# Performance work log

Hardware: AMD Instinct MI355X
Metric: run time of the kernel (lower is better)

## Reference

```python
import jax, jax.numpy as jnp
import numpy as np
import math

N_HEADS = 16


def _rope(t, cos, sin):
    # t: [B, S, H, d_k] with d_k paired as (even, odd) -> complex multiply by cos+i*sin
    B, S, H, dk = t.shape
    t = t.reshape(B, S, H, dk // 2, 2)
    t0, t1 = t[..., 0], t[..., 1]
    c = cos[None, :S, None, :]
    s = sin[None, :S, None, :]
    out = jnp.stack([t0 * c - t1 * s, t0 * s + t1 * c], axis=-1)
    return out.reshape(B, S, H, dk)


def setup_inputs() -> dict:
    key = jax.random.key(0)
    ks = jax.random.split(key, 6)
    B, S, D = 2, 2048, 2048
    dk = D // N_HEADS  # 128
    x = jax.random.normal(ks[0], (B, S, D), dtype=jnp.float32)
    # standard RoPE angle table
    inv_freq = 1.0 / (10000.0 ** (np.arange(0, dk, 2, dtype=np.float32) / dk))  # [dk/2]
    t = np.arange(S, dtype=np.float32)
    ang = np.outer(t, inv_freq)  # [S, dk/2]
    freqs_cos = jnp.asarray(np.cos(ang), dtype=jnp.float32)
    freqs_sin = jnp.asarray(np.sin(ang), dtype=jnp.float32)
    # additive causal mask [1,1,S,S]
    causal = jnp.tril(jnp.ones((S, S), dtype=bool))
    mask = jnp.where(causal, 0.0, -1e9).astype(jnp.float32)[None, None]
    wscale = 1.0 / math.sqrt(D)
    Wq = jax.random.normal(ks[1], (D, D), dtype=jnp.float32) * wscale
    Wk = jax.random.normal(ks[2], (D, D), dtype=jnp.float32) * wscale
    Wv = jax.random.normal(ks[3], (D, D), dtype=jnp.float32) * wscale
    Wo = jax.random.normal(ks[4], (D, D), dtype=jnp.float32) * wscale
    return {"x": x, "freqs_cos": freqs_cos, "freqs_sin": freqs_sin, "mask": mask,
            "Wq": Wq, "Wk": Wk, "Wv": Wv, "Wo": Wo}


def reference(x, freqs_cos, freqs_sin, mask, Wq, Wk, Wv, Wo):
    B, S, D = x.shape
    H = N_HEADS
    dk = D // H
    scale = math.sqrt(dk)
    # nn.Linear(w) applies x @ w.T
    Q = (x @ Wq.T).reshape(B, S, H, dk)
    K = (x @ Wk.T).reshape(B, S, H, dk)
    V = (x @ Wv.T).reshape(B, S, H, dk)
    Q = _rope(Q, freqs_cos, freqs_sin)
    K = _rope(K, freqs_cos, freqs_sin)
    new_kv_cache = (K, V)  # kv_cache=None path: cache is just current K, V
    # [B, H, S, dk]
    Qh = Q.transpose(0, 2, 1, 3)
    Kh = K.transpose(0, 2, 1, 3)
    Vh = V.transpose(0, 2, 1, 3)
    scores = jnp.einsum('bhqd,bhkd->bhqk', Qh, Kh) / scale + mask
    attn = jax.nn.softmax(scores, axis=-1)  # dropout=0 (eval)
    ctx = jnp.einsum('bhqk,bhkd->bhqd', attn, Vh)
    ctx = ctx.transpose(0, 2, 1, 3).reshape(B, S, D)
    output = ctx @ Wo.T
    return output, new_kv_cache[0], new_kv_cache[1]
```

## Files before the change

kernel.cpp:

```cpp
#include <hip/hip_runtime.h>
#include <hip/hip_bf16.h>

#define SEQ   2048
#define DIM   2048
#define NH    16
#define DKH   128
#define BATCH 2
#define MROWS (BATCH * SEQ)
#define NQT   (SEQ / 64)

using bf16 = __hip_bfloat16;
typedef __attribute__((ext_vector_type(8))) short short8;
typedef __attribute__((ext_vector_type(4))) short short4v;
typedef __attribute__((ext_vector_type(4))) float floatx4;

union BfBits { bf16 h; short s; };

__device__ __forceinline__ void gl_lds16(const bf16* g, bf16* l) {
  __builtin_amdgcn_global_load_lds(
      (__attribute__((address_space(1))) void*)(g),
      (__attribute__((address_space(3))) void*)(l), 16, 0, 0);
}

__global__ __launch_bounds__(256) void cast_kernel(const float* __restrict__ src,
                                                   bf16* __restrict__ dst, int n4) {
  int i = blockIdx.x * 256 + threadIdx.x;
  if (i >= n4) return;
  float4 v = reinterpret_cast<const float4*>(src)[i];
  __hip_bfloat162 h01, h23;
  h01.x = __float2bfloat16(v.x); h01.y = __float2bfloat16(v.y);
  h23.x = __float2bfloat16(v.z); h23.y = __float2bfloat16(v.w);
  reinterpret_cast<__hip_bfloat162*>(dst)[i * 2 + 0] = h01;
  reinterpret_cast<__hip_bfloat162*>(dst)[i * 2 + 1] = h23;
}

template <typename CT>
__global__ __launch_bounds__(256) void gemm_bt(const bf16* __restrict__ A,
                                               const bf16* __restrict__ Bw,
                                               CT* __restrict__ C,
                                               int M, int N, int K) {
  __shared__ bf16 As[128 * 32];
  __shared__ bf16 Bs[128 * 32];
  const int t = threadIdx.x;
  const int m0 = blockIdx.y * 128;
  const int n0 = blockIdx.x * 128;
  const int w = t >> 6, lane = t & 63;
  const int wm = (w >> 1) * 64, wn = (w & 1) * 64;
  const int lr = lane & 15, quad = lane >> 4;

  const int c0 = w * 2;
  const int r0 = lane >> 2;
  const int kc = (lane & 3) * 8;

  floatx4 acc[4][4];
#pragma unroll
  for (int i = 0; i < 4; ++i)
#pragma unroll
    for (int j = 0; j < 4; ++j)
      acc[i][j] = (floatx4){0.f, 0.f, 0.f, 0.f};

  for (int k0 = 0; k0 < K; k0 += 32) {
    gl_lds16(A + (size_t)(m0 + c0 * 16 + r0) * K + k0 + kc,       As + c0 * 512);
    gl_lds16(A + (size_t)(m0 + (c0 + 1) * 16 + r0) * K + k0 + kc, As + (c0 + 1) * 512);
    gl_lds16(Bw + (size_t)(n0 + c0 * 16 + r0) * K + k0 + kc,       Bs + c0 * 512);
    gl_lds16(Bw + (size_t)(n0 + (c0 + 1) * 16 + r0) * K + k0 + kc, Bs + (c0 + 1) * 512);
    __syncthreads();

    short8 af[4], bfr[4];
#pragma unroll
    for (int i = 0; i < 4; ++i)
      af[i] = *reinterpret_cast<const short8*>(As + (wm + i * 16 + lr) * 32 + quad * 8);
#pragma unroll
    for (int j = 0; j < 4; ++j)
      bfr[j] = *reinterpret_cast<const short8*>(Bs + (wn + j * 16 + lr) * 32 + quad * 8);
#pragma unroll
    for (int i = 0; i < 4; ++i)
#pragma unroll
      for (int j = 0; j < 4; ++j)
        acc[i][j] = __builtin_amdgcn_mfma_f32_16x16x32_bf16(af[i], bfr[j], acc[i][j], 0, 0, 0);
    __syncthreads();
  }

#pragma unroll
  for (int i = 0; i < 4; ++i)
#pragma unroll
    for (int j = 0; j < 4; ++j) {
      int mrow = m0 + wm + i * 16 + quad * 4;
      int ncol = n0 + wn + j * 16 + lr;
#pragma unroll
      for (int rr = 0; rr < 4; ++rr) {
        if constexpr (__is_same(CT, float))
          C[(size_t)(mrow + rr) * N + ncol] = acc[i][j][rr];
        else
          C[(size_t)(mrow + rr) * N + ncol] = __float2bfloat16(acc[i][j][rr]);
      }
    }
}

__global__ __launch_bounds__(256) void rope_q(const bf16* __restrict__ Qraw,
                                              const float* __restrict__ cosT,
                                              const float* __restrict__ sinT,
                                              bf16* __restrict__ Qb) {
  int g = blockIdx.x * 256 + threadIdx.x;
  int p = g & 63;
  int r = g >> 6;
  int h = r & 15;
  int s = (r >> 4) & (SEQ - 1);
  int b = r >> 15;
  __hip_bfloat162 v = reinterpret_cast<const __hip_bfloat162*>(Qraw)[g];
  float x0 = __bfloat162float(v.x), x1 = __bfloat162float(v.y);
  float c = cosT[s * 64 + p], sn = sinT[s * 64 + p];
  __hip_bfloat162 o;
  o.x = __float2bfloat16(x0 * c - x1 * sn);
  o.y = __float2bfloat16(x0 * sn + x1 * c);
  reinterpret_cast<__hip_bfloat162*>(Qb)[((size_t)(b * NH + h) * SEQ + s) * 64 + p] = o;
}

__global__ __launch_bounds__(256) void rope_k(float* __restrict__ Kf,
                                              const float* __restrict__ cosT,
                                              const float* __restrict__ sinT,
                                              bf16* __restrict__ Kb) {
  int g = blockIdx.x * 256 + threadIdx.x;
  int p = g & 63;
  int r = g >> 6;
  int h = r & 15;
  int s = (r >> 4) & (SEQ - 1);
  int b = r >> 15;
  float2 v = reinterpret_cast<const float2*>(Kf)[g];
  float c = cosT[s * 64 + p], sn = sinT[s * 64 + p];
  float o0 = v.x * c - v.y * sn;
  float o1 = v.x * sn + v.y * c;
  reinterpret_cast<float2*>(Kf)[g] = make_float2(o0, o1);
  __hip_bfloat162 ob;
  ob.x = __float2bfloat16(o0);
  ob.y = __float2bfloat16(o1);
  reinterpret_cast<__hip_bfloat162*>(Kb)[((size_t)(b * NH + h) * SEQ + s) * 64 + p] = ob;
}

__global__ __launch_bounds__(256) void vt_kernel(const float* __restrict__ V,
                                                 bf16* __restrict__ Vt) {
  __shared__ float tile[32][33];
  const int s0 = blockIdx.x * 32;
  const int d0 = blockIdx.y * 32;
  const int bh = blockIdx.z;
  const int b = bh >> 4, h = bh & 15;
  const int t = threadIdx.x;
  const int row = t >> 3, c4 = (t & 7) * 4;

  float4 v = *reinterpret_cast<const float4*>(
      V + (size_t)(b * SEQ + s0 + row) * DIM + h * DKH + d0 + c4);
  tile[row][c4 + 0] = v.x; tile[row][c4 + 1] = v.y;
  tile[row][c4 + 2] = v.z; tile[row][c4 + 3] = v.w;
  __syncthreads();

  short4v ov;
#pragma unroll
  for (int i = 0; i < 4; ++i) {
    BfBits u; u.h = __float2bfloat16(tile[c4 + i][row]);
    ov[i] = u.s;
  }
  *reinterpret_cast<short4v*>(Vt + ((size_t)(b * NH + h) * DKH + d0 + row) * SEQ + s0 + c4) = ov;
}

__global__ __launch_bounds__(256) void attn_mfma(const bf16* __restrict__ Qb,
                                                 const bf16* __restrict__ Kb,
                                                 const bf16* __restrict__ Vt,
                                                 bf16* __restrict__ ctx) {
  const int bx = blockIdx.x;
  const int h = blockIdx.y;
  const int b = blockIdx.z;
  const int t = threadIdx.x;
  const int w = t >> 6, lane = t & 63;
  const int lr = lane & 15, quad = lane >> 4;

  __shared__ short Ks[64 * 136];
  __shared__ short Vs[128 * 72];
  __shared__ short Ps[4 * 16 * 72];

  const float scale = 0.08838834764831845f;
  const size_t headQK = (size_t)(b * NH + h) * SEQ * DKH;

  for (int pass = 0; pass < 2; ++pass) {
    const int qt = pass ? bx : (NQT - 1 - bx);

    short8 qa[4];
    {
      const short* qbase = (const short*)Qb + headQK + (size_t)(qt * 64 + w * 16 + lr) * DKH;
#pragma unroll
      for (int kk = 0; kk < 4; ++kk)
        qa[kk] = *reinterpret_cast<const short8*>(qbase + kk * 32 + quad * 8);
    }

    floatx4 o[8];
#pragma unroll
    for (int n = 0; n < 8; ++n) o[n] = (floatx4){0.f, 0.f, 0.f, 0.f};
    float m[4] = {-1e30f, -1e30f, -1e30f, -1e30f};
    float l[4] = {0.f, 0.f, 0.f, 0.f};

    for (int kt = 0; kt <= qt; ++kt) {
      {
        const short* kbase = (const short*)Kb + headQK + (size_t)(kt * 64) * DKH;
#pragma unroll
        for (int u = 0; u < 4; ++u) {
          int c = t + 256 * u;
          *reinterpret_cast<int4*>(Ks + (c >> 4) * 136 + (c & 15) * 8) =
              *reinterpret_cast<const int4*>(kbase + c * 8);
        }
        const short* vbase = (const short*)Vt + (size_t)(b * NH + h) * DKH * SEQ + kt * 64;
#pragma unroll
        for (int u = 0; u < 4; ++u) {
          int c = t + 256 * u;
          *reinterpret_cast<int4*>(Vs + (c >> 3) * 72 + (c & 7) * 8) =
              *reinterpret_cast<const int4*>(vbase + (size_t)(c >> 3) * SEQ + (c & 7) * 8);
        }
      }
      __syncthreads();

      floatx4 sj[4];
#pragma unroll
      for (int j = 0; j < 4; ++j) sj[j] = (floatx4){0.f, 0.f, 0.f, 0.f};
#pragma unroll
      for (int j = 0; j < 4; ++j)
#pragma unroll
        for (int kk = 0; kk < 4; ++kk) {
          short8 kb = *reinterpret_cast<const short8*>(Ks + (j * 16 + lr) * 136 + kk * 32 + quad * 8);
          sj[j] = __builtin_amdgcn_mfma_f32_16x16x32_bf16(qa[kk], kb, sj[j], 0, 0, 0);
        }

      float sc[4][4];
#pragma unroll
      for (int j = 0; j < 4; ++j)
#pragma unroll
        for (int r = 0; r < 4; ++r) sc[j][r] = sj[j][r] * scale;
      if (kt == qt) {
#pragma unroll
        for (int j = 0; j < 4; ++j) {
          int col = kt * 64 + j * 16 + lr;
#pragma unroll
          for (int r = 0; r < 4; ++r) {
            int rowg = qt * 64 + w * 16 + quad * 4 + r;
            if (col > rowg) sc[j][r] = -1e9f;
          }
        }
      }

#pragma unroll
      for (int r = 0; r < 4; ++r) {
        float mx = fmaxf(fmaxf(sc[0][r], sc[1][r]), fmaxf(sc[2][r], sc[3][r]));
        mx = fmaxf(mx, __shfl_xor(mx, 1, 16));
        mx = fmaxf(mx, __shfl_xor(mx, 2, 16));
        mx = fmaxf(mx, __shfl_xor(mx, 4, 16));
        mx = fmaxf(mx, __shfl_xor(mx, 8, 16));
        float mnew = fmaxf(m[r], mx);
        float alpha = __expf(m[r] - mnew);
        float rs = 0.f;
#pragma unroll
        for (int j = 0; j < 4; ++j) {
          float p = __expf(sc[j][r] - mnew);
          rs += p;
          BfBits u; u.h = __float2bfloat16(p);
          Ps[(w * 16 + quad * 4 + r) * 72 + j * 16 + lr] = u.s;
        }
        rs += __shfl_xor(rs, 1, 16);
        rs += __shfl_xor(rs, 2, 16);
        rs += __shfl_xor(rs, 4, 16);
        rs += __shfl_xor(rs, 8, 16);
        l[r] = l[r] * alpha + rs;
        m[r] = mnew;
#pragma unroll
        for (int n = 0; n < 8; ++n) o[n][r] *= alpha;
      }

      short8 pa0 = *reinterpret_cast<const short8*>(Ps + (w * 16 + lr) * 72 + quad * 8);
      short8 pa1 = *reinterpret_cast<const short8*>(Ps + (w * 16 + lr) * 72 + 32 + quad * 8);
#pragma unroll
      for (int n = 0; n < 8; ++n) {
        short8 vb0 = *reinterpret_cast<const short8*>(Vs + (n * 16 + lr) * 72 + quad * 8);
        short8 vb1 = *reinterpret_cast<const short8*>(Vs + (n * 16 + lr) * 72 + 32 + quad * 8);
        o[n] = __builtin_amdgcn_mfma_f32_16x16x32_bf16(pa0, vb0, o[n], 0, 0, 0);
        o[n] = __builtin_amdgcn_mfma_f32_16x16x32_bf16(pa1, vb1, o[n], 0, 0, 0);
      }
      __syncthreads();
    }

    float inv[4];
#pragma unroll
    for (int r = 0; r < 4; ++r) inv[r] = 1.0f / l[r];
#pragma unroll
    for (int r = 0; r < 4; ++r) {
      size_t mrow = (size_t)b * SEQ + qt * 64 + w * 16 + quad * 4 + r;
      bf16* dst = ctx + mrow * DIM + h * DKH;
#pragma unroll
      for (int n = 0; n < 8; ++n)
        dst[n * 16 + lr] = __float2bfloat16(o[n][r] * inv[r]);
    }
  }
}

extern "C" void kernel_launch(void* const* d_in, const int* in_sizes, int n_in,
                              void* d_out, int out_size, void* d_ws, size_t ws_size,
                              hipStream_t stream) {
  const float* x = (const float*)d_in[0];
  const float* fcos = (const float*)d_in[1];
  const float* fsin = (const float*)d_in[2];
  const float* Wq = (const float*)d_in[4];
  const float* Wk = (const float*)d_in[5];
  const float* Wv = (const float*)d_in[6];
  const float* Wo = (const float*)d_in[7];

  float* out = (float*)d_out;
  float* Kout = out + (size_t)MROWS * DIM;
  float* Vout = Kout + (size_t)MROWS * DIM;

  const size_t MD = (size_t)MROWS * DIM;
  const size_t DD = (size_t)DIM * DIM;
  bf16* xb   = (bf16*)d_ws;
  bf16* Wqb  = xb + MD;
  bf16* Wkb  = Wqb + DD;
  bf16* Wvb  = Wkb + DD;
  bf16* Wob  = Wvb + DD;
  bf16* Qraw = Wob + DD;
  bf16* Qb   = Qraw + MD;
  bf16* Kb   = Qb + MD;
  bf16* Vt   = Kb + MD;
  bf16* ctxb = Qraw;

  const int nXD4 = MROWS * DIM / 4;
  const int nWD4 = DIM * DIM / 4;
  cast_kernel<<<nXD4 / 256, 256, 0, stream>>>(x, xb, nXD4);
  cast_kernel<<<nWD4 / 256, 256, 0, stream>>>(Wq, Wqb, nWD4);
  cast_kernel<<<nWD4 / 256, 256, 0, stream>>>(Wk, Wkb, nWD4);
  cast_kernel<<<nWD4 / 256, 256, 0, stream>>>(Wv, Wvb, nWD4);
  cast_kernel<<<nWD4 / 256, 256, 0, stream>>>(Wo, Wob, nWD4);

  dim3 gg(DIM / 128, MROWS / 128);
  gemm_bt<bf16><<<gg, 256, 0, stream>>>(xb, Wqb, Qraw, MROWS, DIM, DIM);
  gemm_bt<float><<<gg, 256, 0, stream>>>(xb, Wkb, Kout, MROWS, DIM, DIM);
  gemm_bt<float><<<gg, 256, 0, stream>>>(xb, Wvb, Vout, MROWS, DIM, DIM);

  const int npairs = MROWS * DIM / 2;
  rope_q<<<npairs / 256, 256, 0, stream>>>(Qraw, fcos, fsin, Qb);
  rope_k<<<npairs / 256, 256, 0, stream>>>(Kout, fcos, fsin, Kb);

  dim3 gv(SEQ / 32, DKH / 32, BATCH * NH);
  vt_kernel<<<gv, 256, 0, stream>>>(Vout, Vt);

  dim3 ga(NQT / 2, NH, BATCH);
  attn_mfma<<<ga, 256, 0, stream>>>(Qb, Kb, Vt, ctxb);

  gemm_bt<float><<<gg, 256, 0, stream>>>(ctxb, Wob, out, MROWS, DIM, DIM);
}
```

Baseline: 543.0 us.

## Fuse input casts and QKV GEMMs, add lazy-rescale exp2 softmax

Replaces five cast launches with one kernel that converts x and all four weights into one contiguous bf16 buffer. Replaces three projection GEMM launches with a single wide-N GEMM that reads the concatenated Wq/Wk/Wv and routes each output tile to Q, K or V. Attention now works in base 2 with exp2, and only rescales the running max and accumulators when the row max grows past a threshold. This cuts launch count and per-tile exp/rescale work, in exchange for a larger fused grid and softmax values that may exceed one before normalisation.

```diff
diff --git a/kernel.cpp b/kernel.cpp
--- a/kernel.cpp
+++ b/kernel.cpp
@@ -22,16 +22,94 @@
       (__attribute__((address_space(3))) void*)(l), 16, 0, 0);
 }
 
-__global__ __launch_bounds__(256) void cast_kernel(const float* __restrict__ src,
-                                                   bf16* __restrict__ dst, int n4) {
+__global__ __launch_bounds__(256) void cast5_kernel(const float* __restrict__ x,
+                                                    const float* __restrict__ wq,
+                                                    const float* __restrict__ wk,
+                                                    const float* __restrict__ wv,
+                                                    const float* __restrict__ wo,
+                                                    bf16* __restrict__ dst,
+                                                    int nX4, int nW4, int nTot) {
   int i = blockIdx.x * 256 + threadIdx.x;
-  if (i >= n4) return;
-  float4 v = reinterpret_cast<const float4*>(src)[i];
+  if (i >= nTot) return;
+  const float* src;
+  int off;
+  int j = i - nX4;
+  if (j < 0) { src = x; off = i; }
+  else {
+    int wsel = j >> 20;
+    off = j & (nW4 - 1);
+    src = (wsel == 0) ? wq : (wsel == 1) ? wk : (wsel == 2) ? wv : wo;
+  }
+  float4 v = reinterpret_cast<const float4*>(src)[off];
   __hip_bfloat162 h01, h23;
   h01.x = __float2bfloat16(v.x); h01.y = __float2bfloat16(v.y);
   h23.x = __float2bfloat16(v.z); h23.y = __float2bfloat16(v.w);
   reinterpret_cast<__hip_bfloat162*>(dst)[i * 2 + 0] = h01;
   reinterpret_cast<__hip_bfloat162*>(dst)[i * 2 + 1] = h23;
+}
+
+__global__ __launch_bounds__(256) void gemm_qkv(const bf16* __restrict__ A,
+                                                const bf16* __restrict__ Bw,
+                                                bf16* __restrict__ Qraw,
+                                                float* __restrict__ Kout,
+                                                float* __restrict__ Vout) {
+  __shared__ bf16 As[128 * 32];
+  __shared__ bf16 Bs[128 * 32];
+  const int t = threadIdx.x;
+  const int m0 = blockIdx.y * 128;
+  const int n0 = blockIdx.x * 128;
+  const int w = t >> 6, lane = t & 63;
+  const int wm = (w >> 1) * 64, wn = (w & 1) * 64;
+  const int lr = lane & 15, quad = lane >> 4;
+
+  const int c0 = w * 2;
+  const int r0 = lane >> 2;
+  const int kc = (lane & 3) * 8;
+
+  floatx4 acc[4][4];
+#pragma unroll
+  for (int i = 0; i < 4; ++i)
+#pragma unroll
+    for (int j = 0; j < 4; ++j)
+      acc[i][j] = (floatx4){0.f, 0.f, 0.f, 0.f};
+
+  for (int k0 = 0; k0 < DIM; k0 += 32) {
+    gl_lds16(A + (size_t)(m0 + c0 * 16 + r0) * DIM + k0 + kc,       As + c0 * 512);
+    gl_lds16(A + (size_t)(m0 + (c0 + 1) * 16 + r0) * DIM + k0 + kc, As + (c0 + 1) * 512);
+    gl_lds16(Bw + (size_t)(n0 + c0 * 16 + r0) * DIM + k0 + kc,       Bs + c0 * 512);
+    gl_lds16(Bw + (size_t)(n0 + (c0 + 1) * 16 + r0) * DIM + k0 + kc, Bs + (c0 + 1) * 512);
+    __syncthreads();
+
+    short8 af[4], bfr[4];
+#pragma unroll
+    for (int i = 0; i < 4; ++i)
+      af[i] = *reinterpret_cast<const short8*>(As + (wm + i * 16 + lr) * 32 + quad * 8);
+#pragma unroll
+    for (int j = 0; j < 4; ++j)
+      bfr[j] = *reinterpret_cast<const short8*>(Bs + (wn + j * 16 + lr) * 32 + quad * 8);
+#pragma unroll
+    for (int i = 0; i < 4; ++i)
+#pragma unroll
+      for (int j = 0; j < 4; ++j)
+        acc[i][j] = __builtin_amdgcn_mfma_f32_16x16x32_bf16(af[i], bfr[j], acc[i][j], 0, 0, 0);
+    __syncthreads();
+  }
+
+  const int region = n0 >> 11;
+#pragma unroll
+  for (int i = 0; i < 4; ++i)
+#pragma unroll
+    for (int j = 0; j < 4; ++j) {
+      int mrow = m0 + wm + i * 16 + quad * 4;
+      int lcol = (n0 & 2047) + wn + j * 16 + lr;
+#pragma unroll
+      for (int rr = 0; rr < 4; ++rr) {
+        size_t idx = (size_t)(mrow + rr) * DIM + lcol;
+        if (region == 0)      Qraw[idx] = __float2bfloat16(acc[i][j][rr]);
+        else if (region == 1) Kout[idx] = acc[i][j][rr];
+        else                  Vout[idx] = acc[i][j][rr];
+      }
+    }
 }
 
 template <typename CT>
@@ -177,7 +255,8 @@
   __shared__ short Vs[128 * 72];
   __shared__ short Ps[4 * 16 * 72];
 
-  const float scale = 0.08838834764831845f;
+  const float scale2 = 0.08838834764831845f * 1.44269504f;
+  const float THR = 11.5413f;
   const size_t headQK = (size_t)(b * NH + h) * SEQ * DKH;
 
   for (int pass = 0; pass < 2; ++pass) {
@@ -231,7 +310,7 @@
 #pragma unroll
       for (int j = 0; j < 4; ++j)
 #pragma unroll
-        for (int r = 0; r < 4; ++r) sc[j][r] = sj[j][r] * scale;
+        for (int r = 0; r < 4; ++r) sc[j][r] = sj[j][r] * scale2;
       if (kt == qt) {
 #pragma unroll
         for (int j = 0; j < 4; ++j) {
@@ -251,12 +330,18 @@
         mx = fmaxf(mx, __shfl_xor(mx, 2, 16));
         mx = fmaxf(mx, __shfl_xor(mx, 4, 16));
         mx = fmaxf(mx, __shfl_xor(mx, 8, 16));
-        float mnew = fmaxf(m[r], mx);
-        float alpha = __expf(m[r] - mnew);
+        if (!__all(mx - m[r] <= THR)) {
+          float mnew = fmaxf(m[r], mx);
+          float alpha = __builtin_amdgcn_exp2f(m[r] - mnew);
+          l[r] *= alpha;
+#pragma unroll
+          for (int n = 0; n < 8; ++n) o[n][r] *= alpha;
+          m[r] = mnew;
+        }
         float rs = 0.f;
 #pragma unroll
         for (int j = 0; j < 4; ++j) {
-          float p = __expf(sc[j][r] - mnew);
+          float p = __builtin_amdgcn_exp2f(sc[j][r] - m[r]);
           rs += p;
           BfBits u; u.h = __float2bfloat16(p);
           Ps[(w * 16 + quad * 4 + r) * 72 + j * 16 + lr] = u.s;
@@ -265,10 +350,7 @@
         rs += __shfl_xor(rs, 2, 16);
         rs += __shfl_xor(rs, 4, 16);
         rs += __shfl_xor(rs, 8, 16);
-        l[r] = l[r] * alpha + rs;
-        m[r] = mnew;
-#pragma unroll
-        for (int n = 0; n < 8; ++n) o[n][r] *= alpha;
+        l[r] += rs;
       }
 
       short8 pa0 = *reinterpret_cast<const short8*>(Ps + (w * 16 + lr) * 72 + quad * 8);
@@ -327,16 +409,11 @@
 
   const int nXD4 = MROWS * DIM / 4;
   const int nWD4 = DIM * DIM / 4;
-  cast_kernel<<<nXD4 / 256, 256, 0, stream>>>(x, xb, nXD4);
-  cast_kernel<<<nWD4 / 256, 256, 0, stream>>>(Wq, Wqb, nWD4);
-  cast_kernel<<<nWD4 / 256, 256, 0, stream>>>(Wk, Wkb, nWD4);
-  cast_kernel<<<nWD4 / 256, 256, 0, stream>>>(Wv, Wvb, nWD4);
-  cast_kernel<<<nWD4 / 256, 256, 0, stream>>>(Wo, Wob, nWD4);
-
-  dim3 gg(DIM / 128, MROWS / 128);
-  gemm_bt<bf16><<<gg, 256, 0, stream>>>(xb, Wqb, Qraw, MROWS, DIM, DIM);
-  gemm_bt<float><<<gg, 256, 0, stream>>>(xb, Wkb, Kout, MROWS, DIM, DIM);
-  gemm_bt<float><<<gg, 256, 0, stream>>>(xb, Wvb, Vout, MROWS, DIM, DIM);
+  const int nTot = nXD4 + 4 * nWD4;
+  cast5_kernel<<<nTot / 256, 256, 0, stream>>>(x, Wq, Wk, Wv, Wo, xb, nXD4, nWD4, nTot);
+
+  dim3 gq(3 * DIM / 128, MROWS / 128);
+  gemm_qkv<<<gq, 256, 0, stream>>>(xb, Wqb, Qraw, Kout, Vout);
 
   const int npairs = MROWS * DIM / 2;
   rope_q<<<npairs / 256, 256, 0, stream>>>(Qraw, fcos, fsin, Qb);
@@ -348,5 +425,6 @@
   dim3 ga(NQT / 2, NH, BATCH);
   attn_mfma<<<ga, 256, 0, stream>>>(Qb, Kb, Vt, ctxb);
 
+  dim3 gg(DIM / 128, MROWS / 128);
   gemm_bt<float><<<gg, 256, 0, stream>>>(ctxb, Wob, out, MROWS, DIM, DIM);
 }
```

Measured after the change: 520.2 us. -4.2%, faster.
